# Performance work log

Hardware: AMD Instinct MI355X
Metric: run time of the kernel (lower is better)

Reference implementation:

```python
import jax, jax.numpy as jnp
import numpy as np

B, N, DIM, H, DH, K = 2, 2048, 512, 8, 64, 32
SCALE = DH ** -0.5


def setup_inputs() -> dict:
    key = jax.random.key(0)
    ks = jax.random.split(key, 9)
    return {
        "x": jax.random.normal(ks[0], (B, N, DIM), jnp.float32),
        "mem_kv": jax.random.normal(ks[1], (B, H, N, K, 2, DH), jnp.float32),
        "mem_mask": jax.random.bernoulli(ks[2], 0.9, (B, H, N, K)),
        "Wq": jax.random.normal(ks[3], (DIM, H * DH), jnp.float32) * (DIM ** -0.5),
        "Wkv": jax.random.normal(ks[4], (DIM, 2 * DH), jnp.float32) * (DIM ** -0.5),
        "Wo": jax.random.normal(ks[5], (H * DH, DIM), jnp.float32) * ((H * DH) ** -0.5),
        "bo": jnp.zeros((DIM,), jnp.float32),
        "null_k": jax.random.normal(ks[6], (DH,), jnp.float32),
        "null_v": jax.random.normal(ks[7], (DH,), jnp.float32),
        "gate": jax.random.normal(ks[8], (H, 1, 1), jnp.float32),
    }


def reference(x, mem_kv, mem_mask, Wq, Wkv, Wo, bo, null_k, null_v, gate):
    b, n, _ = x.shape
    mask_value = -jnp.finfo(x.dtype).max

    # projections
    q = (x @ Wq).reshape(b, n, H, DH).transpose(0, 2, 1, 3)  # b h n d
    kv = x @ Wkv                                             # b n 2d
    k, v = kv[..., :DH], kv[..., DH:]                        # b n d (shared kv head)

    # local causal attention
    sim = jnp.einsum('bhid,bjd->bhij', q, k) * SCALE
    causal = jnp.triu(jnp.ones((n, n), bool), 1)
    sim = jnp.where(causal, mask_value, sim)
    attn = jax.nn.softmax(sim, axis=-1)
    local_values = jnp.einsum('bhij,bjd->bhid', attn, v)

    # kNN memory attention (retrieved keys/values are per-query)
    mem_k, mem_v = mem_kv[..., 0, :], mem_kv[..., 1, :]      # b h n k d
    nk = jnp.broadcast_to(null_k, (b, H, n, 1, DH))
    nv = jnp.broadcast_to(null_v, (b, H, n, 1, DH))
    mem_k = jnp.concatenate([nk, mem_k], axis=-2)
    mem_v = jnp.concatenate([nv, mem_v], axis=-2)
    mmask = jnp.concatenate([jnp.ones((b, H, n, 1), bool), mem_mask], axis=-1)

    sim_mem = jnp.einsum('bhid,bhijd->bhij', q, mem_k) * SCALE
    sim_mem = jnp.where(mmask, sim_mem, mask_value)
    attn_mem = jax.nn.softmax(sim_mem, axis=-1)
    mem_values = jnp.einsum('bhij,bhijd->bhid', attn_mem, mem_v)

    # gated combine of the two attention paths
    g = jax.nn.sigmoid(gate)                                 # h 1 1
    out = local_values * g + mem_values * (1.0 - g)          # b h n d
    out = out.transpose(0, 2, 1, 3).reshape(b, n, H * DH)
    return out @ Wo + bo
```

## Files before the change

kernel.cpp:

```cpp
#include <hip/hip_runtime.h>
#include <cstddef>
#include <cstdint>

#define SEQ_N  2048
#define NHEAD  8
#define DHEAD  64
#define NMEM   32
#define SCALE_F 0.125f
#define NEG_INF -3.0e38f
#define LDK 72

typedef short bf16x8 __attribute__((ext_vector_type(8)));
typedef float f32x4  __attribute__((ext_vector_type(4)));

__device__ __forceinline__ unsigned short f2bf(float f) {
  union { float f; uint32_t u; } v; v.f = f;
  uint32_t u = v.u;
  return (unsigned short)((u + 0x7fffu + ((u >> 16) & 1u)) >> 16);
}
__device__ __forceinline__ float bf2f(unsigned short us) {
  union { uint32_t u; float f; } v; v.u = ((uint32_t)us) << 16; return v.f;
}

__device__ __forceinline__ float wred_max(float v) {
#pragma unroll
  for (int o = 32; o > 0; o >>= 1) v = fmaxf(v, __shfl_xor(v, o));
  return v;
}
__device__ __forceinline__ float wred_sum(float v) {
#pragma unroll
  for (int o = 32; o > 0; o >>= 1) v += __shfl_xor(v, o);
  return v;
}

template <int MODE>
__global__ __launch_bounds__(256) void gemm64(
    const float* __restrict__ A, const float* __restrict__ Bw,
    float* __restrict__ Cf, unsigned short* __restrict__ Ck,
    unsigned short* __restrict__ Cv,
    const float* __restrict__ bias, int Kdim, int Ncols) {
  __shared__ float sA[64][17];
  __shared__ float sB[16][64];
  const int tid = threadIdx.x;
  const int tx = tid & 15, ty = tid >> 4;
  const int rowBase = blockIdx.x * 64, colBase = blockIdx.y * 64;
  float acc[4][4] = {};

  for (int k0 = 0; k0 < Kdim; k0 += 16) {
    {
      int r = tid >> 2, ks = (tid & 3) * 4;
      float4 a4 = *(const float4*)(A + (size_t)(rowBase + r) * Kdim + k0 + ks);
      sA[r][ks + 0] = a4.x; sA[r][ks + 1] = a4.y;
      sA[r][ks + 2] = a4.z; sA[r][ks + 3] = a4.w;
    }
#pragma unroll
    for (int it = 0; it < 4; ++it) {
      int kk = (tid >> 6) + it * 4, c = tid & 63;
      sB[kk][c] = Bw[(size_t)(k0 + kk) * Ncols + colBase + c];
    }
    __syncthreads();
#pragma unroll
    for (int kk = 0; kk < 16; ++kk) {
      float av[4];
#pragma unroll
      for (int u = 0; u < 4; ++u) av[u] = sA[ty * 4 + u][kk];
      float4 b4 = *(const float4*)&sB[kk][tx * 4];
#pragma unroll
      for (int u = 0; u < 4; ++u) {
        acc[u][0] += av[u] * b4.x; acc[u][1] += av[u] * b4.y;
        acc[u][2] += av[u] * b4.z; acc[u][3] += av[u] * b4.w;
      }
    }
    __syncthreads();
  }

#pragma unroll
  for (int ri = 0; ri < 4; ++ri) {
    int r = rowBase + ty * 4 + ri;
#pragma unroll
    for (int ci = 0; ci < 4; ++ci) {
      int c = colBase + tx * 4 + ci;
      float val = acc[ri][ci];
      if (MODE == 0) {
        int b = r >> 11, i = r & 2047, h = c >> 6, d = c & 63;
        Ck[(((size_t)(b * NHEAD + h)) * SEQ_N + i) * DHEAD + d] =
            f2bf(val * SCALE_F);
      } else if (MODE == 1) {
        if (c < DHEAD) {
          Ck[(size_t)r * DHEAD + c] = f2bf(val);
        } else {
          int b = r >> 11, i = r & 2047, d = c - DHEAD;
          Cv[((size_t)b * DHEAD + d) * SEQ_N + i] = f2bf(val);
        }
      } else {
        Cf[(size_t)r * 512 + c] = val + bias[c];
      }
    }
  }
}

__global__ __launch_bounds__(256) void mem_attn_kernel(
    const unsigned short* __restrict__ qb, const float* __restrict__ mem_kv,
    const int* __restrict__ mem_mask, const float* __restrict__ null_k,
    const float* __restrict__ null_v, float* __restrict__ mem_out) {
  __shared__ float sq[4][64];
  const int w = threadIdx.x >> 6;
  const int lane = threadIdx.x & 63;
  const int row = blockIdx.x * 4 + w;
  const float qv = bf2f(qb[(size_t)row * DHEAD + lane]);
  sq[w][lane] = qv;
  __syncthreads();

  const float* mk = mem_kv + (size_t)row * (NMEM * 2 * DHEAD);

  float nullsim = wred_sum(qv * null_k[lane]);

  float sim = NEG_INF;
  if (lane == 0) {
    sim = nullsim;
  } else if (lane <= NMEM) {
    int j = lane - 1;
    const float4* kp = (const float4*)(mk + j * 2 * DHEAD);
    float s = 0.f;
#pragma unroll
    for (int d4 = 0; d4 < 16; ++d4) {
      float4 k4 = kp[d4];
      float4 q4 = *(const float4*)&sq[w][d4 * 4];
      s += k4.x * q4.x + k4.y * q4.y + k4.z * q4.z + k4.w * q4.w;
    }
    if (mem_mask[(size_t)row * NMEM + j] == 0) s = NEG_INF;
    sim = s;
  }

  float m = wred_max(sim);
  float p = __expf(sim - m);
  if (lane > NMEM) p = 0.f;
  float l = wred_sum(p);
  p /= l;

  float acc = __shfl(p, 0) * null_v[lane];
#pragma unroll
  for (int j = 0; j < NMEM; ++j) {
    float pj = __shfl(p, j + 1);
    acc += pj * mk[j * 2 * DHEAD + DHEAD + lane];
  }
  mem_out[(size_t)row * DHEAD + lane] = acc;
}

__global__ __launch_bounds__(256) void local_attn_mfma(
    const unsigned short* __restrict__ qb, const unsigned short* __restrict__ kb,
    const unsigned short* __restrict__ vtb, const float* __restrict__ mem_o,
    const float* __restrict__ gate, float* __restrict__ comb) {
  __shared__ unsigned short sK[64 * LDK];
  __shared__ unsigned short sV[64 * LDK];
  __shared__ unsigned short sP[4 * 16 * LDK];

  const int tid = threadIdx.x;
  const int w = tid >> 6, lane = tid & 63;
  const int m = lane & 15, quad = lane >> 4;
  const int bid = blockIdx.x;
  const int qt = 31 - (bid >> 4);
  const int bh = bid & 15;
  const int b = bh >> 3, h = bh & 7;
  const int qbase = qt * 64;

  const unsigned short* qp =
      qb + (((size_t)bh * SEQ_N + qbase + w * 16 + m) * DHEAD) + quad * 8;
  const bf16x8 aq0 = *(const bf16x8*)qp;
  const bf16x8 aq1 = *(const bf16x8*)(qp + 32);

  f32x4 acc[4] = {};
  float mrow[4], lrow[4];
#pragma unroll
  for (int r = 0; r < 4; ++r) { mrow[r] = NEG_INF; lrow[r] = 0.f; }

  unsigned short* sPw = &sP[w * 16 * LDK];

  for (int kt = 0; kt <= qt; ++kt) {
    const int kbase0 = kt * 64;
    __syncthreads();
#pragma unroll
    for (int it = 0; it < 2; ++it) {
      int idx = tid + it * 256;
      int row = idx >> 3, ch = idx & 7;
      *(uint4*)&sK[row * LDK + ch * 8] =
          *(const uint4*)(kb + ((size_t)b * SEQ_N + kbase0 + row) * DHEAD + ch * 8);
      *(uint4*)&sV[row * LDK + ch * 8] =
          *(const uint4*)(vtb + ((size_t)b * DHEAD + row) * SEQ_N + kbase0 + ch * 8);
    }
    __syncthreads();

    f32x4 s[4] = {};
#pragma unroll
    for (int nb = 0; nb < 4; ++nb) {
      bf16x8 bk0 = *(const bf16x8*)&sK[(nb * 16 + m) * LDK + quad * 8];
      bf16x8 bk1 = *(const bf16x8*)&sK[(nb * 16 + m) * LDK + 32 + quad * 8];
      s[nb] = __builtin_amdgcn_mfma_f32_16x16x32_bf16(aq0, bk0, s[nb], 0, 0, 0);
      s[nb] = __builtin_amdgcn_mfma_f32_16x16x32_bf16(aq1, bk1, s[nb], 0, 0, 0);
    }

    if (kt == qt) {
      int irow0 = w * 16 + quad * 4;
#pragma unroll
      for (int nb = 0; nb < 4; ++nb) {
        int j = nb * 16 + m;
#pragma unroll
        for (int r = 0; r < 4; ++r)
          if (j > irow0 + r) s[nb][r] = NEG_INF;
      }
    }

#pragma unroll
    for (int r = 0; r < 4; ++r) {
      float mx = fmaxf(fmaxf(s[0][r], s[1][r]), fmaxf(s[2][r], s[3][r]));
      mx = fmaxf(mx, __shfl_xor(mx, 1));
      mx = fmaxf(mx, __shfl_xor(mx, 2));
      mx = fmaxf(mx, __shfl_xor(mx, 4));
      mx = fmaxf(mx, __shfl_xor(mx, 8));
      float mnew = fmaxf(mrow[r], mx);
      float alpha = __expf(mrow[r] - mnew);
      mrow[r] = mnew;
      float rs = 0.f;
#pragma unroll
      for (int nb = 0; nb < 4; ++nb) {
        float p = __expf(s[nb][r] - mnew);
        s[nb][r] = p;
        rs += p;
      }
      rs += __shfl_xor(rs, 1); rs += __shfl_xor(rs, 2);
      rs += __shfl_xor(rs, 4); rs += __shfl_xor(rs, 8);
      lrow[r] = lrow[r] * alpha + rs;
#pragma unroll
      for (int db = 0; db < 4; ++db) acc[db][r] *= alpha;
    }

#pragma unroll
    for (int nb = 0; nb < 4; ++nb)
#pragma unroll
      for (int r = 0; r < 4; ++r)
        sPw[(quad * 4 + r) * LDK + nb * 16 + m] = f2bf(s[nb][r]);

    bf16x8 ap0 = *(const bf16x8*)&sPw[m * LDK + quad * 8];
    bf16x8 ap1 = *(const bf16x8*)&sPw[m * LDK + 32 + quad * 8];

#pragma unroll
    for (int db = 0; db < 4; ++db) {
      bf16x8 bv0 = *(const bf16x8*)&sV[(db * 16 + m) * LDK + quad * 8];
      bf16x8 bv1 = *(const bf16x8*)&sV[(db * 16 + m) * LDK + 32 + quad * 8];
      acc[db] = __builtin_amdgcn_mfma_f32_16x16x32_bf16(ap0, bv0, acc[db], 0, 0, 0);
      acc[db] = __builtin_amdgcn_mfma_f32_16x16x32_bf16(ap1, bv1, acc[db], 0, 0, 0);
    }
  }

  const float g = 1.f / (1.f + __expf(-gate[h]));
#pragma unroll
  for (int r = 0; r < 4; ++r) {
    int i = qbase + w * 16 + quad * 4 + r;
    float invl = 1.f / lrow[r];
#pragma unroll
    for (int db = 0; db < 4; ++db) {
      int d = db * 16 + m;
      float localv = acc[db][r] * invl;
      float memv = mem_o[((size_t)bh * SEQ_N + i) * DHEAD + d];
      comb[((size_t)(b * SEQ_N + i)) * 512 + h * DHEAD + d] =
          g * localv + (1.f - g) * memv;
    }
  }
}

extern "C" void kernel_launch(void* const* d_in, const int* in_sizes, int n_in,
                              void* d_out, int out_size, void* d_ws, size_t ws_size,
                              hipStream_t stream) {
  const float* x        = (const float*)d_in[0];
  const float* mem_kv   = (const float*)d_in[1];
  const int*   mem_mask = (const int*)d_in[2];
  const float* Wq       = (const float*)d_in[3];
  const float* Wkv      = (const float*)d_in[4];
  const float* Wo       = (const float*)d_in[5];
  const float* bo       = (const float*)d_in[6];
  const float* null_k   = (const float*)d_in[7];
  const float* null_v   = (const float*)d_in[8];
  const float* gate     = (const float*)d_in[9];
  float* out = (float*)d_out;

  unsigned short* qb  = (unsigned short*)d_ws;
  unsigned short* kbw = qb + 2097152;
  unsigned short* vtb = kbw + 262144;
  float* mem_o = (float*)(vtb + 262144);
  float* comb  = mem_o + 2097152;

  dim3 blk(256);
  gemm64<0><<<dim3(64, 8), blk, 0, stream>>>(x, Wq, nullptr, qb, nullptr, nullptr, 512, 512);
  gemm64<1><<<dim3(64, 2), blk, 0, stream>>>(x, Wkv, nullptr, kbw, vtb, nullptr, 512, 128);
  mem_attn_kernel<<<8192, blk, 0, stream>>>(qb, mem_kv, mem_mask, null_k, null_v, mem_o);
  local_attn_mfma<<<512, blk, 0, stream>>>(qb, kbw, vtb, mem_o, gate, comb);
  gemm64<2><<<dim3(64, 8), blk, 0, stream>>>(comb, Wo, out, nullptr, nullptr, bo, 512, 512);
}
```

Before: 887.0 us.

## Restructure memory attention kernel for coalesced float4 loads and register-resident KV

Rewrites the kNN memory attention kernel so each 16-lane group reads contiguous float4 chunks of four memory keys/values at once. All 32 keys and values for a row are held in registers, and dot products are reduced with xor-shuffles. This replaces the old pattern where each lane strided through one key's 64 floats and V was read serially over 32 iterations. The goal is fully coalesced, high-bandwidth reads of the large mem_kv tensor and the removal of shared memory and the block barrier, at the cost of more registers and more shuffle operations.

```diff
diff --git a/kernel.cpp b/kernel.cpp
--- a/kernel.cpp
+++ b/kernel.cpp
@@ -103,48 +103,79 @@
     const unsigned short* __restrict__ qb, const float* __restrict__ mem_kv,
     const int* __restrict__ mem_mask, const float* __restrict__ null_k,
     const float* __restrict__ null_v, float* __restrict__ mem_out) {
-  __shared__ float sq[4][64];
   const int w = threadIdx.x >> 6;
   const int lane = threadIdx.x & 63;
   const int row = blockIdx.x * 4 + w;
-  const float qv = bf2f(qb[(size_t)row * DHEAD + lane]);
-  sq[w][lane] = qv;
-  __syncthreads();
+  const int g = lane >> 4;
+  const int t = lane & 15;
 
   const float* mk = mem_kv + (size_t)row * (NMEM * 2 * DHEAD);
 
-  float nullsim = wred_sum(qv * null_k[lane]);
-
-  float sim = NEG_INF;
-  if (lane == 0) {
-    sim = nullsim;
-  } else if (lane <= NMEM) {
-    int j = lane - 1;
-    const float4* kp = (const float4*)(mk + j * 2 * DHEAD);
-    float s = 0.f;
-#pragma unroll
-    for (int d4 = 0; d4 < 16; ++d4) {
-      float4 k4 = kp[d4];
-      float4 q4 = *(const float4*)&sq[w][d4 * 4];
-      s += k4.x * q4.x + k4.y * q4.y + k4.z * q4.z + k4.w * q4.w;
-    }
-    if (mem_mask[(size_t)row * NMEM + j] == 0) s = NEG_INF;
-    sim = s;
-  }
-
-  float m = wred_max(sim);
-  float p = __expf(sim - m);
-  if (lane > NMEM) p = 0.f;
-  float l = wred_sum(p);
-  p /= l;
-
-  float acc = __shfl(p, 0) * null_v[lane];
-#pragma unroll
-  for (int j = 0; j < NMEM; ++j) {
-    float pj = __shfl(p, j + 1);
-    acc += pj * mk[j * 2 * DHEAD + DHEAD + lane];
-  }
-  mem_out[(size_t)row * DHEAD + lane] = acc;
+  ushort4 qu = *(const ushort4*)(qb + (size_t)row * DHEAD + t * 4);
+  float4 nk4 = *(const float4*)(null_k + t * 4);
+  float4 nv4 = *(const float4*)(null_v + t * 4);
+  int mymask = (lane < NMEM) ? mem_mask[(size_t)row * NMEM + lane] : 1;
+
+  float4 k4[8], v4[8];
+#pragma unroll
+  for (int i = 0; i < 8; ++i) {
+    const float* kj = mk + (size_t)(i * 4 + g) * (2 * DHEAD);
+    k4[i] = *(const float4*)(kj + t * 4);
+    v4[i] = *(const float4*)(kj + DHEAD + t * 4);
+  }
+
+  const float q0 = bf2f(qu.x), q1 = bf2f(qu.y);
+  const float q2 = bf2f(qu.z), q3 = bf2f(qu.w);
+
+  float nsim = q0 * nk4.x + q1 * nk4.y + q2 * nk4.z + q3 * nk4.w;
+  nsim += __shfl_xor(nsim, 1); nsim += __shfl_xor(nsim, 2);
+  nsim += __shfl_xor(nsim, 4); nsim += __shfl_xor(nsim, 8);
+
+  float s[8];
+#pragma unroll
+  for (int i = 0; i < 8; ++i) {
+    float sv = q0 * k4[i].x + q1 * k4[i].y + q2 * k4[i].z + q3 * k4[i].w;
+    sv += __shfl_xor(sv, 1); sv += __shfl_xor(sv, 2);
+    sv += __shfl_xor(sv, 4); sv += __shfl_xor(sv, 8);
+    int mj = __shfl(mymask, i * 4 + g);
+    s[i] = (mj == 0) ? NEG_INF : sv;
+  }
+
+  float mloc = nsim;
+#pragma unroll
+  for (int i = 0; i < 8; ++i) mloc = fmaxf(mloc, s[i]);
+  mloc = fmaxf(mloc, __shfl_xor(mloc, 16));
+  mloc = fmaxf(mloc, __shfl_xor(mloc, 32));
+
+  float p[8];
+  float psum = 0.f;
+#pragma unroll
+  for (int i = 0; i < 8; ++i) { p[i] = __expf(s[i] - mloc); psum += p[i]; }
+  psum += __shfl_xor(psum, 16);
+  psum += __shfl_xor(psum, 32);
+  const float pn = __expf(nsim - mloc);
+  const float linv = 1.f / (pn + psum);
+
+  float ax = 0.f, ay = 0.f, az = 0.f, aw = 0.f;
+#pragma unroll
+  for (int i = 0; i < 8; ++i) {
+    float pj = p[i] * linv;
+    ax += pj * v4[i].x; ay += pj * v4[i].y;
+    az += pj * v4[i].z; aw += pj * v4[i].w;
+  }
+  ax += __shfl_xor(ax, 16); ay += __shfl_xor(ay, 16);
+  az += __shfl_xor(az, 16); aw += __shfl_xor(aw, 16);
+  ax += __shfl_xor(ax, 32); ay += __shfl_xor(ay, 32);
+  az += __shfl_xor(az, 32); aw += __shfl_xor(aw, 32);
+
+  const float pnl = pn * linv;
+  ax += pnl * nv4.x; ay += pnl * nv4.y;
+  az += pnl * nv4.z; aw += pnl * nv4.w;
+
+  if (g == 0) {
+    float4 o = {ax, ay, az, aw};
+    *(float4*)(mem_out + (size_t)row * DHEAD + t * 4) = o;
+  }
 }
 
 __global__ __launch_bounds__(256) void local_attn_mfma(
```

Result: no change. 888.4 us (+0.2%).
